# Kernel optimization log

Measured on AMD Instinct MI355X. Metric: run time of the kernel, lower is better.

The kernel has to match this reference:

```python
import jax, jax.numpy as jnp
import numpy as np

INPUT_SIZE = 16
K = 50
HIDDEN_COUNT = 25
FINAL_WIDTH = INPUT_SIZE + HIDDEN_COUNT * K  # 1266


def setup_inputs() -> dict:
    key = jax.random.key(0)
    k1, k2, k3, k4, k5 = jax.random.split(key, 5)
    B = 32768
    state = jax.random.normal(k1, (B, INPUT_SIZE), dtype=jnp.float32)
    # Zero-padded weight stack: layer i uses Ws[i, :, : INPUT_SIZE + i*K]
    Ws = jax.random.normal(k2, (HIDDEN_COUNT, K, FINAL_WIDTH), dtype=jnp.float32) * 0.05
    bs = jax.random.normal(k3, (HIDDEN_COUNT, K), dtype=jnp.float32) * 0.05
    Wout = jax.random.normal(k4, (FINAL_WIDTH, 1), dtype=jnp.float32) * 0.05
    bout = jax.random.normal(k5, (1,), dtype=jnp.float32) * 0.05
    return {"state": state, "Ws": Ws, "bs": bs, "Wout": Wout, "bout": bout}


def reference(state, Ws, bs, Wout, bout):
    x = state  # [B, 16], grows by 50 per layer
    for i in range(HIDDEN_COUNT):  # fixed-size structural loop over layers
        width = INPUT_SIZE + i * K
        w = Ws[i, :, :width]                       # [50, width] (static slice)
        y = jax.nn.leaky_relu(x @ w.T + bs[i], negative_slope=0.01)  # [B, 50]
        x = jnp.concatenate([x, y], axis=1)        # [B, width+50]
    return x @ Wout + bout  # [B, 1]
```

## Files before the change

kernel.cpp:

```cpp
#include <hip/hip_runtime.h>


#define IN 16
#define KJ 50
#define NL 25
#define FW 1266
#define TR 24
#define NB 1366
#define BTOT 32768
#define XSTR 1272
#define NTHREADS 1024
#define XLO_OFF 61056
#define SLAB_OFF 122112
#define BIAS_OFF 154880
#define LDS_BYTES 159880
#define CHUNK_STRIDE 3200
#define TOTAL_CHUNKS 973

typedef __attribute__((ext_vector_type(8))) short bf16x8;
typedef __attribute__((ext_vector_type(16))) float f32x16;

__device__ __forceinline__ unsigned short bf16_hi(float x, float* hif) {
    unsigned u = __float_as_uint(x);
    unsigned h = (u + 0x8000u) >> 16;
    *hif = __uint_as_float(h << 16);
    return (unsigned short)h;
}
__device__ __forceinline__ unsigned short bf16_rnd(float x) {
    return (unsigned short)((__float_as_uint(x) + 0x8000u) >> 16);
}

__device__ __forceinline__ void split8(const float* __restrict__ rowp, int kb, int width,
                                       unsigned hi[4], unsigned lo[4]) {
#pragma unroll
    for (int p = 0; p < 4; ++p) {
        unsigned h2[2], l2[2];
#pragma unroll
        for (int q = 0; q < 2; ++q) {
            int k = kb + p * 2 + q;
            float v = (k < width) ? rowp[k] : 0.f;
            float hif;
            unsigned short h = bf16_hi(v, &hif);
            h2[q] = h;
            l2[q] = bf16_rnd(v - hif);
        }
        hi[p] = h2[0] | (h2[1] << 16);
        lo[p] = l2[0] | (l2[1] << 16);
    }
}

__global__ __launch_bounds__(64, 1) void split_w(const float* __restrict__ Ws,
                                                 char* __restrict__ wsbuf) {
    int rem = blockIdx.x, layer = 0;
    size_t off = 0;
    for (;;) {
        int c = (IN + KJ * layer + 15) >> 4;
        if (rem < c) break;
        rem -= c; off += (size_t)c * CHUNK_STRIDE; ++layer;
    }
    const int ci = rem, k0 = ci << 4, width = IN + KJ * layer;
    const float* Wl = Ws + (size_t)layer * KJ * FW;
    char* base = wsbuf + off + (size_t)ci * CHUNK_STRIDE;
    const int l = threadIdx.x, ll = l & 31, kh = l >> 5;
    const int kb = k0 + kh * 8;

    unsigned hi[4], lo[4];
    split8(Wl + (size_t)ll * FW, kb, width, hi, lo);
    *reinterpret_cast<uint4*>(base + l * 16)        = make_uint4(hi[0], hi[1], hi[2], hi[3]);
    *reinterpret_cast<uint4*>(base + 1024 + l * 16) = make_uint4(lo[0], lo[1], lo[2], lo[3]);
    if (ll < 18) {
        split8(Wl + (size_t)(32 + ll) * FW, kb, width, hi, lo);
        *reinterpret_cast<uint4*>(base + 2048 + (kh * 18 + ll) * 16) = make_uint4(hi[0], hi[1], hi[2], hi[3]);
        *reinterpret_cast<uint4*>(base + 2624 + (kh * 18 + ll) * 16) = make_uint4(lo[0], lo[1], lo[2], lo[3]);
    }
}

__device__ __forceinline__ void loadB2(const char* __restrict__ wb, int ci, int chunks,
                                       int n, int l, int ll, int kh,
                                       bf16x8& bh, bf16x8& bl) {
    bf16x8 z = {0, 0, 0, 0, 0, 0, 0, 0};
    bh = z; bl = z;
    if (ci < chunks) {
        const char* cb = wb + (size_t)ci * CHUNK_STRIDE;
        if (n == 0) {
            bh = *(const bf16x8*)(cb + l * 16);
            bl = *(const bf16x8*)(cb + 1024 + l * 16);
        } else if (ll < 18) {
            bh = *(const bf16x8*)(cb + (kh * 18 + ll) * 16);
            bl = *(const bf16x8*)(cb + 576 + (kh * 18 + ll) * 16);
        }
    }
}

__device__ __forceinline__ void mfma3(const unsigned short* xrh, const unsigned short* xrl,
                                      int kof, const bf16x8 bh, const bf16x8 bl, f32x16& acc) {
    bf16x8 ah = *(const bf16x8*)(xrh + kof);
    bf16x8 al = *(const bf16x8*)(xrl + kof);
    acc = __builtin_amdgcn_mfma_f32_32x32x16_bf16(al, bh, acc, 0, 0, 0);
    acc = __builtin_amdgcn_mfma_f32_32x32x16_bf16(ah, bl, acc, 0, 0, 0);
    acc = __builtin_amdgcn_mfma_f32_32x32x16_bf16(ah, bh, acc, 0, 0, 0);
}

__global__ __launch_bounds__(NTHREADS, 4) void densenet_mfma(
    const float* __restrict__ state, const char* __restrict__ wsbuf,
    const float* __restrict__ bs,    const float* __restrict__ Wout,
    const float* __restrict__ bout,  float* __restrict__ out)
{
    __shared__ __align__(16) char lds[LDS_BYTES];
    unsigned short* xhi = (unsigned short*)lds;
    unsigned short* xlo = (unsigned short*)(lds + XLO_OFF);
    float* slab  = (float*)(lds + SLAB_OFF);
    float* biasl = (float*)(lds + BIAS_OFF);

    const int tid = threadIdx.x;
    const int w   = tid >> 6;
    const int l   = tid & 63;
    const int ll  = l & 31, kh = l >> 5;
    const int kq  = w & 7;
    const int n   = w >> 3;
    const long row0 = (long)blockIdx.x * TR;

    {
        unsigned* p = (unsigned*)lds;
        for (int i = tid; i < SLAB_OFF / 4; i += NTHREADS) p[i] = 0u;
    }
    for (int i = tid; i < NL * KJ; i += NTHREADS) biasl[i] = bs[i];
    __syncthreads();
    if (tid < TR * IN) {
        int r = tid >> 4, c = tid & 15;
        if (row0 + r < BTOT) {
            float v = state[(row0 + r) * IN + c];
            float hif;
            xhi[r * XSTR + c] = bf16_hi(v, &hif);
            xlo[r * XSTR + c] = bf16_rnd(v - hif);
        }
    }
    __syncthreads();

    const unsigned short* xrh = xhi + ll * XSTR + (kh << 3);
    const unsigned short* xrl = xlo + ll * XSTR + (kh << 3);

    int width = IN;
    size_t wofs = 0;
    for (int layer = 0; layer < NL; ++layer) {
        const int chunks = (width + 15) >> 4;
        const char* wb = wsbuf + wofs + (n ? 2048 : 0);

        f32x16 a0, a1;
#pragma unroll
        for (int i = 0; i < 16; ++i) { a0[i] = 0.f; a1[i] = 0.f; }

        bf16x8 A0h, A0l, A1h, A1l, B0h, B0l, B1h, B1l;
        loadB2(wb, kq,     chunks, n, l, ll, kh, A0h, A0l);
        loadB2(wb, kq + 8, chunks, n, l, ll, kh, A1h, A1l);
        for (int c0 = kq; c0 < chunks; c0 += 32) {
            loadB2(wb, c0 + 16, chunks, n, l, ll, kh, B0h, B0l);
            loadB2(wb, c0 + 24, chunks, n, l, ll, kh, B1h, B1l);
            mfma3(xrh, xrl, c0 << 4, A0h, A0l, a0);
            if (c0 + 8 < chunks)  mfma3(xrh, xrl, (c0 + 8) << 4, A1h, A1l, a1);
            if (c0 + 32 < chunks) {
                loadB2(wb, c0 + 32, chunks, n, l, ll, kh, A0h, A0l);
                loadB2(wb, c0 + 40, chunks, n, l, ll, kh, A1h, A1l);
            }
            if (c0 + 16 < chunks) mfma3(xrh, xrl, (c0 + 16) << 4, B0h, B0l, a0);
            if (c0 + 24 < chunks) mfma3(xrh, xrl, (c0 + 24) << 4, B1h, B1l, a1);
        }

        {
            float* s1 = slab + kq * 1024 + n * 32 + ll;
#pragma unroll
            for (int r = 0; r < 8; ++r) {
                int crow = (r & 3) + 8 * (r >> 2) + 4 * kh;
                s1[crow * 64] = a0[r] + a1[r];
            }
        }
        __syncthreads();
        {
            int row = tid >> 6, j = tid & 63;
            float s = 0.f;
#pragma unroll
            for (int q = 0; q < 8; ++q) s += slab[q * 1024 + row * 64 + j];
            if (j < KJ) {
                s += biasl[layer * KJ + j];
                s = (s > 0.f) ? s : 0.01f * s;
                float hif;
                xhi[row * XSTR + width + j] = bf16_hi(s, &hif);
                xlo[row * XSTR + width + j] = bf16_rnd(s - hif);
            }
        }
        __syncthreads();
        {
            float* s2 = slab + kq * 512 + n * 32 + ll;
#pragma unroll
            for (int r = 0; r < 4; ++r) {
                int lrow = (r & 3) + 4 * kh;
                s2[lrow * 64] = a0[8 + r] + a1[8 + r];
            }
        }
        __syncthreads();
        if (tid < 512) {
            int lrow = tid >> 6, j = tid & 63;
            int row = 16 + lrow;
            float s = 0.f;
#pragma unroll
            for (int q = 0; q < 8; ++q) s += slab[q * 512 + lrow * 64 + j];
            if (j < KJ) {
                s += biasl[layer * KJ + j];
                s = (s > 0.f) ? s : 0.01f * s;
                float hif;
                xhi[row * XSTR + width + j] = bf16_hi(s, &hif);
                xlo[row * XSTR + width + j] = bf16_rnd(s - hif);
            }
        }
        __syncthreads();

        width += KJ;
        wofs += (size_t)chunks * CHUNK_STRIDE;
    }

    const float b0 = bout[0];
#pragma unroll
    for (int rr = 0; rr < 2; ++rr) {
        if (rr == 1 && w >= 8) break;
        const int row = rr ? 16 + w : w;
        const long grow = row0 + row;
        const unsigned short* xh = xhi + row * XSTR;
        const unsigned short* xl = xlo + row * XSTR;
        float s = 0.f;
#pragma unroll
        for (int it = 0; it < 19; ++it) {
            int k = l + (it << 6);
            float xv = __uint_as_float((unsigned)xh[k] << 16)
                     + __uint_as_float((unsigned)xl[k] << 16);
            s += xv * Wout[k];
        }
        {
            int k = 1216 + l;
            if (k < FW) {
                float xv = __uint_as_float((unsigned)xh[k] << 16)
                         + __uint_as_float((unsigned)xl[k] << 16);
                s += xv * Wout[k];
            }
        }
#pragma unroll
        for (int m = 32; m >= 1; m >>= 1) s += __shfl_xor(s, m, 64);
        if (l == 0 && grow < BTOT) out[grow] = s + b0;
    }
}

extern "C" void kernel_launch(void* const* d_in, const int* in_sizes, int n_in,
                              void* d_out, int out_size, void* d_ws, size_t ws_size,
                              hipStream_t stream) {
    const float* state = (const float*)d_in[0];
    const float* Ws    = (const float*)d_in[1];
    const float* bs    = (const float*)d_in[2];
    const float* Wout  = (const float*)d_in[3];
    const float* bout  = (const float*)d_in[4];
    float* out = (float*)d_out;
    char* wsbuf = (char*)d_ws;

    split_w<<<dim3(TOTAL_CHUNKS), dim3(64), 0, stream>>>(Ws, wsbuf);
    densenet_mfma<<<dim3(NB), dim3(NTHREADS), 0, stream>>>(state, wsbuf, bs, Wout, bout, out);
}
```

Before: 500.5 us.

## Overlap next layer's fully-ready K chunks with current layer's reduction barriers

Each layer's GEMM is split in two. Chunks whose input columns already existed before the previous layer are computed early, during the previous layer's epilogue, into a second set of accumulators. Only the chunks that depend on the newly produced columns are computed after the barriers. Double-buffered accumulators, swapped through a macro unrolled twice per iteration, let MFMA work fill the time before the slab/syncthreads reduction. This raises register pressure, with 64 accumulator floats live under a 1024-thread, 4-wave-per-SIMD launch bound, which risks spills and adds code size.

```diff
diff --git a/kernel.cpp b/kernel.cpp
--- a/kernel.cpp
+++ b/kernel.cpp
@@ -75,12 +75,12 @@
     }
 }
 
-__device__ __forceinline__ void loadB2(const char* __restrict__ wb, int ci, int chunks,
+__device__ __forceinline__ void loadB2(const char* __restrict__ wb, int ci, int bound,
                                        int n, int l, int ll, int kh,
                                        bf16x8& bh, bf16x8& bl) {
     bf16x8 z = {0, 0, 0, 0, 0, 0, 0, 0};
     bh = z; bl = z;
-    if (ci < chunks) {
+    if (ci < bound) {
         const char* cb = wb + (size_t)ci * CHUNK_STRIDE;
         if (n == 0) {
             bh = *(const bf16x8*)(cb + l * 16);
@@ -99,6 +99,90 @@
     acc = __builtin_amdgcn_mfma_f32_32x32x16_bf16(al, bh, acc, 0, 0, 0);
     acc = __builtin_amdgcn_mfma_f32_32x32x16_bf16(ah, bl, acc, 0, 0, 0);
     acc = __builtin_amdgcn_mfma_f32_32x32x16_bf16(ah, bh, acc, 0, 0, 0);
+}
+
+#define BODY(CUR0, CUR1, NXT0, NXT1, LAST)                                      \
+{                                                                               \
+    const int chunks = (width + 15) >> 4;                                       \
+    const char* wb = wsbuf + wofs + (n ? 2048 : 0);                             \
+              \
+    {                                                                           \
+        int ci = bnd + ((kq - bnd) & 7);                                        \
+        for (; ci < chunks; ci += 8) {                                          \
+            bf16x8 tbh, tbl;                                                    \
+            loadB2(wb, ci, chunks, n, l, ll, kh, tbh, tbl);                     \
+            mfma3(xrh, xrl, ci << 4, tbh, tbl, CUR0);                           \
+        }                                                                       \
+    }                                                                           \
+      \
+    {                                                                           \
+        float* s1 = slab + kq * 1024 + n * 32 + ll;                             \
+        _Pragma("unroll")                                                       \
+        for (int r = 0; r < 8; ++r) {                                           \
+            int crow = (r & 3) + 8 * (r >> 2) + 4 * kh;                         \
+            s1[crow * 64] = CUR0[r] + CUR1[r];                                  \
+        }                                                                       \
+    }                                                                           \
+        \
+           \
+    if (!LAST) {                                                                \
+        _Pragma("unroll")                                                       \
+        for (int z = 0; z < 16; ++z) { NXT0[z] = 0.f; NXT1[z] = 0.f; }          \
+        const int hbnd = width >> 4;                                            \
+        const char* nwb = wb + (size_t)chunks * CHUNK_STRIDE;                   \
+        bf16x8 A0h, A0l, A1h, A1l;                                              \
+        loadB2(nwb, kq,     hbnd, n, l, ll, kh, A0h, A0l);                      \
+        loadB2(nwb, kq + 8, hbnd, n, l, ll, kh, A1h, A1l);                      \
+        for (int c0 = kq; c0 < hbnd; c0 += 16) {                                \
+            mfma3(xrh, xrl, c0 << 4, A0h, A0l, NXT0);                           \
+            if (c0 + 16 < hbnd) loadB2(nwb, c0 + 16, hbnd, n, l, ll, kh, A0h, A0l); \
+            if (c0 + 8 < hbnd)  mfma3(xrh, xrl, (c0 + 8) << 4, A1h, A1l, NXT1); \
+            if (c0 + 24 < hbnd) loadB2(nwb, c0 + 24, hbnd, n, l, ll, kh, A1h, A1l); \
+        }                                                                       \
+    }                                                                           \
+    __syncthreads();               \
+    {                               \
+        int row = tid >> 6, j = tid & 63;                                       \
+        float s = 0.f;                                                          \
+        _Pragma("unroll")                                                       \
+        for (int q = 0; q < 8; ++q) s += slab[q * 1024 + row * 64 + j];         \
+        if (j < KJ) {                                                           \
+            s += biasl[lidx * KJ + j];                                          \
+            s = (s > 0.f) ? s : 0.01f * s;                                      \
+            float hif;                                                          \
+            xhi[row * XSTR + width + j] = bf16_hi(s, &hif);                     \
+            xlo[row * XSTR + width + j] = bf16_rnd(s - hif);                    \
+        }                                                                       \
+    }                                                                           \
+    __syncthreads();             \
+    {                        \
+        float* s2 = slab + kq * 512 + n * 32 + ll;                              \
+        _Pragma("unroll")                                                       \
+        for (int r = 0; r < 4; ++r) {                                           \
+            int lrow = (r & 3) + 4 * kh;                                        \
+            s2[lrow * 64] = CUR0[8 + r] + CUR1[8 + r];                          \
+        }                                                                       \
+    }                                                                           \
+    __syncthreads();                                                   \
+    if (tid < 512) {                                                            \
+        int lrow = tid >> 6, j = tid & 63;                                      \
+        int row = 16 + lrow;                                                    \
+        float s = 0.f;                                                          \
+        _Pragma("unroll")                                                       \
+        for (int q = 0; q < 8; ++q) s += slab[q * 512 + lrow * 64 + j];         \
+        if (j < KJ) {                                                           \
+            s += biasl[lidx * KJ + j];                                          \
+            s = (s > 0.f) ? s : 0.01f * s;                                      \
+            float hif;                                                          \
+            xhi[row * XSTR + width + j] = bf16_hi(s, &hif);                     \
+            xlo[row * XSTR + width + j] = bf16_rnd(s - hif);                    \
+        }                                                                       \
+    }                                                                           \
+    __syncthreads();                     \
+    bnd = width >> 4;                                                           \
+    width += KJ;                                                                \
+    wofs += (size_t)chunks * CHUNK_STRIDE;                                      \
+    ++lidx;                                                                     \
 }
 
 __global__ __launch_bounds__(NTHREADS, 4) void densenet_mfma(
@@ -140,83 +224,17 @@
     const unsigned short* xrh = xhi + ll * XSTR + (kh << 3);
     const unsigned short* xrl = xlo + ll * XSTR + (kh << 3);
 
-    int width = IN;
+    f32x16 cA0, cA1, nA0, nA1;
+#pragma unroll
+    for (int i = 0; i < 16; ++i) { cA0[i] = 0.f; cA1[i] = 0.f; nA0[i] = 0.f; nA1[i] = 0.f; }
+
+    int lidx = 0, width = IN, bnd = 0;
     size_t wofs = 0;
-    for (int layer = 0; layer < NL; ++layer) {
-        const int chunks = (width + 15) >> 4;
-        const char* wb = wsbuf + wofs + (n ? 2048 : 0);
-
-        f32x16 a0, a1;
-#pragma unroll
-        for (int i = 0; i < 16; ++i) { a0[i] = 0.f; a1[i] = 0.f; }
-
-        bf16x8 A0h, A0l, A1h, A1l, B0h, B0l, B1h, B1l;
-        loadB2(wb, kq,     chunks, n, l, ll, kh, A0h, A0l);
-        loadB2(wb, kq + 8, chunks, n, l, ll, kh, A1h, A1l);
-        for (int c0 = kq; c0 < chunks; c0 += 32) {
-            loadB2(wb, c0 + 16, chunks, n, l, ll, kh, B0h, B0l);
-            loadB2(wb, c0 + 24, chunks, n, l, ll, kh, B1h, B1l);
-            mfma3(xrh, xrl, c0 << 4, A0h, A0l, a0);
-            if (c0 + 8 < chunks)  mfma3(xrh, xrl, (c0 + 8) << 4, A1h, A1l, a1);
-            if (c0 + 32 < chunks) {
-                loadB2(wb, c0 + 32, chunks, n, l, ll, kh, A0h, A0l);
-                loadB2(wb, c0 + 40, chunks, n, l, ll, kh, A1h, A1l);
-            }
-            if (c0 + 16 < chunks) mfma3(xrh, xrl, (c0 + 16) << 4, B0h, B0l, a0);
-            if (c0 + 24 < chunks) mfma3(xrh, xrl, (c0 + 24) << 4, B1h, B1l, a1);
-        }
-
-        {
-            float* s1 = slab + kq * 1024 + n * 32 + ll;
-#pragma unroll
-            for (int r = 0; r < 8; ++r) {
-                int crow = (r & 3) + 8 * (r >> 2) + 4 * kh;
-                s1[crow * 64] = a0[r] + a1[r];
-            }
-        }
-        __syncthreads();
-        {
-            int row = tid >> 6, j = tid & 63;
-            float s = 0.f;
-#pragma unroll
-            for (int q = 0; q < 8; ++q) s += slab[q * 1024 + row * 64 + j];
-            if (j < KJ) {
-                s += biasl[layer * KJ + j];
-                s = (s > 0.f) ? s : 0.01f * s;
-                float hif;
-                xhi[row * XSTR + width + j] = bf16_hi(s, &hif);
-                xlo[row * XSTR + width + j] = bf16_rnd(s - hif);
-            }
-        }
-        __syncthreads();
-        {
-            float* s2 = slab + kq * 512 + n * 32 + ll;
-#pragma unroll
-            for (int r = 0; r < 4; ++r) {
-                int lrow = (r & 3) + 4 * kh;
-                s2[lrow * 64] = a0[8 + r] + a1[8 + r];
-            }
-        }
-        __syncthreads();
-        if (tid < 512) {
-            int lrow = tid >> 6, j = tid & 63;
-            int row = 16 + lrow;
-            float s = 0.f;
-#pragma unroll
-            for (int q = 0; q < 8; ++q) s += slab[q * 512 + lrow * 64 + j];
-            if (j < KJ) {
-                s += biasl[layer * KJ + j];
-                s = (s > 0.f) ? s : 0.01f * s;
-                float hif;
-                xhi[row * XSTR + width + j] = bf16_hi(s, &hif);
-                xlo[row * XSTR + width + j] = bf16_rnd(s - hif);
-            }
-        }
-        __syncthreads();
-
-        width += KJ;
-        wofs += (size_t)chunks * CHUNK_STRIDE;
-    }
+    for (int ip = 0; ip < 12; ++ip) {
+        BODY(cA0, cA1, nA0, nA1, 0)
+        BODY(nA0, nA1, cA0, cA1, 0)
+    }
+    BODY(cA0, cA1, nA0, nA1, 1)
 
     const float b0 = bout[0];
 #pragma unroll
```

After: 488.2 us. 1.03x faster.

## Pad weight chunks to uniform layout and split MFMA chains across three accumulators

Applied to the files above, without the earlier changes.

Pads each packed weight chunk to a 4 KB stride so both column halves use the same lane-uniform 16-byte loads, removing the n/ll branching in the B-fragment loads. The inner K loop is restructured into a four-deep software pipeline that prefetches both weight fragments and LDS activation fragments ahead of use. The three bf16 hi/lo product MFMAs now go into separate accumulators, which breaks the serial dependency chain between them. The cost is more global memory traffic from zero padding (the second half's 576-byte region becomes 1024 bytes), plus extra registers for the third accumulator and the deeper prefetch, which may pressure occupancy at 1024 threads.

```diff
diff --git a/kernel.cpp b/kernel.cpp
--- a/kernel.cpp
+++ b/kernel.cpp
@@ -14,7 +14,6 @@
 #define SLAB_OFF 122112
 #define BIAS_OFF 154880
 #define LDS_BYTES 159880
-#define CHUNK_STRIDE 3200
 #define TOTAL_CHUNKS 973
 
 typedef __attribute__((ext_vector_type(8))) short bf16x8;
@@ -56,11 +55,11 @@
     for (;;) {
         int c = (IN + KJ * layer + 15) >> 4;
         if (rem < c) break;
-        rem -= c; off += (size_t)c * CHUNK_STRIDE; ++layer;
+        rem -= c; off += (size_t)c << 12; ++layer;
     }
     const int ci = rem, k0 = ci << 4, width = IN + KJ * layer;
     const float* Wl = Ws + (size_t)layer * KJ * FW;
-    char* base = wsbuf + off + (size_t)ci * CHUNK_STRIDE;
+    char* base = wsbuf + off + ((size_t)ci << 12);
     const int l = threadIdx.x, ll = l & 31, kh = l >> 5;
     const int kb = k0 + kh * 8;
 
@@ -68,38 +67,29 @@
     split8(Wl + (size_t)ll * FW, kb, width, hi, lo);
     *reinterpret_cast<uint4*>(base + l * 16)        = make_uint4(hi[0], hi[1], hi[2], hi[3]);
     *reinterpret_cast<uint4*>(base + 1024 + l * 16) = make_uint4(lo[0], lo[1], lo[2], lo[3]);
+    uint4 zh = make_uint4(0u, 0u, 0u, 0u), zl = zh;
     if (ll < 18) {
         split8(Wl + (size_t)(32 + ll) * FW, kb, width, hi, lo);
-        *reinterpret_cast<uint4*>(base + 2048 + (kh * 18 + ll) * 16) = make_uint4(hi[0], hi[1], hi[2], hi[3]);
-        *reinterpret_cast<uint4*>(base + 2624 + (kh * 18 + ll) * 16) = make_uint4(lo[0], lo[1], lo[2], lo[3]);
-    }
-}
-
-__device__ __forceinline__ void loadB2(const char* __restrict__ wb, int ci, int chunks,
-                                       int n, int l, int ll, int kh,
-                                       bf16x8& bh, bf16x8& bl) {
-    bf16x8 z = {0, 0, 0, 0, 0, 0, 0, 0};
-    bh = z; bl = z;
-    if (ci < chunks) {
-        const char* cb = wb + (size_t)ci * CHUNK_STRIDE;
-        if (n == 0) {
-            bh = *(const bf16x8*)(cb + l * 16);
-            bl = *(const bf16x8*)(cb + 1024 + l * 16);
-        } else if (ll < 18) {
-            bh = *(const bf16x8*)(cb + (kh * 18 + ll) * 16);
-            bl = *(const bf16x8*)(cb + 576 + (kh * 18 + ll) * 16);
-        }
-    }
-}
-
-__device__ __forceinline__ void mfma3(const unsigned short* xrh, const unsigned short* xrl,
-                                      int kof, const bf16x8 bh, const bf16x8 bl, f32x16& acc) {
-    bf16x8 ah = *(const bf16x8*)(xrh + kof);
-    bf16x8 al = *(const bf16x8*)(xrl + kof);
-    acc = __builtin_amdgcn_mfma_f32_32x32x16_bf16(al, bh, acc, 0, 0, 0);
-    acc = __builtin_amdgcn_mfma_f32_32x32x16_bf16(ah, bl, acc, 0, 0, 0);
-    acc = __builtin_amdgcn_mfma_f32_32x32x16_bf16(ah, bh, acc, 0, 0, 0);
-}
+        zh = make_uint4(hi[0], hi[1], hi[2], hi[3]);
+        zl = make_uint4(lo[0], lo[1], lo[2], lo[3]);
+    }
+    *reinterpret_cast<uint4*>(base + 2048 + l * 16) = zh;
+    *reinterpret_cast<uint4*>(base + 3072 + l * 16) = zl;
+}
+
+#define LB(S, CI) { bf16x8 z_ = {0,0,0,0,0,0,0,0}; S##h = z_; S##l = z_;           \
+    if ((CI) < chunks) { const char* cb_ = wb + ((size_t)(CI) << 12);              \
+        S##h = *(const bf16x8*)(cb_ + l16);                                        \
+        S##l = *(const bf16x8*)(cb_ + 1024 + l16); } }
+
+#define LA(S, CI) if ((CI) < chunks) { const int kof_ = (CI) << 4;                 \
+    S##h = *(const bf16x8*)(xrh + kof_);                                           \
+    S##l = *(const bf16x8*)(xrl + kof_); }
+
+#define MF3(S, T) {                                                                \
+    aP = __builtin_amdgcn_mfma_f32_32x32x16_bf16(S##l, T##h, aP, 0, 0, 0);         \
+    aQ = __builtin_amdgcn_mfma_f32_32x32x16_bf16(S##h, T##l, aQ, 0, 0, 0);         \
+    aR = __builtin_amdgcn_mfma_f32_32x32x16_bf16(S##h, T##h, aR, 0, 0, 0); }
 
 __global__ __launch_bounds__(NTHREADS, 4) void densenet_mfma(
     const float* __restrict__ state, const char* __restrict__ wsbuf,
@@ -116,6 +106,7 @@
     const int w   = tid >> 6;
     const int l   = tid & 63;
     const int ll  = l & 31, kh = l >> 5;
+    const int l16 = l << 4;
     const int kq  = w & 7;
     const int n   = w >> 3;
     const long row0 = (long)blockIdx.x * TR;
@@ -146,24 +137,24 @@
         const int chunks = (width + 15) >> 4;
         const char* wb = wsbuf + wofs + (n ? 2048 : 0);
 
-        f32x16 a0, a1;
-#pragma unroll
-        for (int i = 0; i < 16; ++i) { a0[i] = 0.f; a1[i] = 0.f; }
-
-        bf16x8 A0h, A0l, A1h, A1l, B0h, B0l, B1h, B1l;
-        loadB2(wb, kq,     chunks, n, l, ll, kh, A0h, A0l);
-        loadB2(wb, kq + 8, chunks, n, l, ll, kh, A1h, A1l);
+        f32x16 aP, aQ, aR;
+#pragma unroll
+        for (int i = 0; i < 16; ++i) { aP[i] = 0.f; aQ[i] = 0.f; aR[i] = 0.f; }
+
+        bf16x8 zz = {0,0,0,0,0,0,0,0};
+        bf16x8 A0h = zz, A0l = zz, A1h = zz, A1l = zz;
+        bf16x8 B0h, B0l, B1h, B1l, B2h, B2l, B3h, B3l;
+        LB(B0, kq) LB(B1, kq + 8) LB(B2, kq + 16) LB(B3, kq + 24)
+        LA(A0, kq) LA(A1, kq + 8)
         for (int c0 = kq; c0 < chunks; c0 += 32) {
-            loadB2(wb, c0 + 16, chunks, n, l, ll, kh, B0h, B0l);
-            loadB2(wb, c0 + 24, chunks, n, l, ll, kh, B1h, B1l);
-            mfma3(xrh, xrl, c0 << 4, A0h, A0l, a0);
-            if (c0 + 8 < chunks)  mfma3(xrh, xrl, (c0 + 8) << 4, A1h, A1l, a1);
-            if (c0 + 32 < chunks) {
-                loadB2(wb, c0 + 32, chunks, n, l, ll, kh, A0h, A0l);
-                loadB2(wb, c0 + 40, chunks, n, l, ll, kh, A1h, A1l);
-            }
-            if (c0 + 16 < chunks) mfma3(xrh, xrl, (c0 + 16) << 4, B0h, B0l, a0);
-            if (c0 + 24 < chunks) mfma3(xrh, xrl, (c0 + 24) << 4, B1h, B1l, a1);
+            MF3(A0, B0)
+            LA(A0, c0 + 16) LB(B0, c0 + 32)
+            if (c0 + 8 < chunks) { MF3(A1, B1) }
+            LA(A1, c0 + 24) LB(B1, c0 + 40)
+            if (c0 + 16 < chunks) { MF3(A0, B2) }
+            LA(A0, c0 + 32) LB(B2, c0 + 48)
+            if (c0 + 24 < chunks) { MF3(A1, B3) }
+            LA(A1, c0 + 40) LB(B3, c0 + 56)
         }
 
         {
@@ -171,7 +162,7 @@
 #pragma unroll
             for (int r = 0; r < 8; ++r) {
                 int crow = (r & 3) + 8 * (r >> 2) + 4 * kh;
-                s1[crow * 64] = a0[r] + a1[r];
+                s1[crow * 64] = (aP[r] + aQ[r]) + aR[r];
             }
         }
         __syncthreads();
@@ -194,7 +185,7 @@
 #pragma unroll
             for (int r = 0; r < 4; ++r) {
                 int lrow = (r & 3) + 4 * kh;
-                s2[lrow * 64] = a0[8 + r] + a1[8 + r];
+                s2[lrow * 64] = (aP[8 + r] + aQ[8 + r]) + aR[8 + r];
             }
         }
         __syncthreads();
@@ -215,7 +206,7 @@
         __syncthreads();
 
         width += KJ;
-        wofs += (size_t)chunks * CHUNK_STRIDE;
+        wofs += (size_t)chunks << 12;
     }
 
     const float b0 = bout[0];
```

After: 773.0 us. 54.4% more time.
